# Kernel tuning notes

Hardware: AMD Instinct MI355X
Metric: run time of the kernel (lower is better)

## Reference

```python
import jax, jax.numpy as jnp
import numpy as np


def _conv1x1(x, w, b):
    # x: [B, Cin, H, W], w: [Cout, Cin], b: [Cout]
    return jnp.einsum('bchw,oc->bohw', x, w) + b[None, :, None, None]


def setup_inputs() -> dict:
    key = jax.random.key(0)
    ks = jax.random.split(key, 9)
    B, C, H, W = 32, 512, 32, 32
    Cout, dn = 512, 512
    s_in = 1.0 / np.sqrt(C)
    s_out = 1.0 / np.sqrt(Cout)
    return {
        'x': jax.random.normal(ks[0], (B, C, H, W), jnp.float32),
        'wA': jax.random.uniform(ks[1], (Cout, C), jnp.float32, -s_in, s_in),
        'bA': jax.random.uniform(ks[2], (Cout,), jnp.float32, -s_in, s_in),
        'wB': jax.random.uniform(ks[3], (dn, C), jnp.float32, -s_in, s_in),
        'bB': jax.random.uniform(ks[4], (dn,), jnp.float32, -s_in, s_in),
        'wV': jax.random.uniform(ks[5], (dn, C), jnp.float32, -s_in, s_in),
        'bV': jax.random.uniform(ks[6], (dn,), jnp.float32, -s_in, s_in),
        'wR': jax.random.uniform(ks[7], (Cout, Cout), jnp.float32, -s_out, s_out),
        'bR': jax.random.uniform(ks[8], (Cout,), jnp.float32, -s_out, s_out),
    }


def reference(x, wA, bA, wB, bB, wV, bV, wR, bR):
    Bsz, C, H, W = x.shape
    Cout = wA.shape[0]
    A = _conv1x1(x, wA, bA).reshape(Bsz, Cout, H * W)          # [B, Cout, N]
    Bm = _conv1x1(x, wB, bB).reshape(Bsz, wB.shape[0], H * W)  # [B, dn, N]
    Vm = _conv1x1(x, wV, bV).reshape(Bsz, wV.shape[0], H * W)  # [B, dn, N]
    attn_maps = jax.nn.softmax(Bm, axis=-1)                    # softmax over spatial
    attn_vectors = jax.nn.softmax(Vm, axis=-1)                 # softmax over spatial
    glob_desc = jnp.einsum('bcn,bdn->bcd', A, attn_maps)       # [B, Cout, dn]
    Z = jnp.einsum('bcd,bdn->bcn', glob_desc, attn_vectors)    # [B, Cout, N]
    Z = Z.reshape(Bsz, Cout, H, W)
    Z = _conv1x1(Z, wR, bR)
    return Z
```

## Files before the change

kernel.cpp:

```cpp
#include <hip/hip_runtime.h>
#include <stdint.h>

typedef unsigned short u16;
typedef __bf16  bf16x8 __attribute__((ext_vector_type(8)));
typedef float   f32x4  __attribute__((ext_vector_type(4)));

__device__ __forceinline__ u16 f2bf(float f) {
    union { float f; unsigned u; } c; c.f = f;
    unsigned r = c.u + 0x7fffu + ((c.u >> 16) & 1u);
    return (u16)(r >> 16);
}
__device__ __forceinline__ float bf2f(u16 b) {
    union { unsigned u; float f; } c; c.u = ((unsigned)b) << 16; return c.f;
}

__device__ __forceinline__ void g2l16(const u16* g, u16* l) {
    __builtin_amdgcn_global_load_lds(
        (__attribute__((address_space(1))) void*)(uintptr_t)g,
        (__attribute__((address_space(3))) void*)(uint32_t)(uintptr_t)l,
        16, 0, 0);
}

template <int TM, bool HAS_BIAS, bool OUT_F32, bool EPI>
__device__ __forceinline__ void gemm_core(
    const u16* __restrict__ Ab, const u16* __restrict__ Bb, void* __restrict__ C,
    const float* __restrict__ bias, int N, int K, long cbase, int m0, int n0,
    const float* __restrict__ svec, const float* __restrict__ wRbA)
{
    constexpr int MI = TM / 32;
    constexpr int NA = TM / 32;
    __shared__ __align__(16) u16 As[TM * 64];
    __shared__ __align__(16) u16 Bs[128 * 64];

    const int t = threadIdx.x;
    const int w = t >> 6, lane = t & 63;
    const int wr = w >> 1, wc = w & 1;

    f32x4 acc[MI][4];
    const f32x4 zero = {0.f, 0.f, 0.f, 0.f};
#pragma unroll
    for (int i = 0; i < MI; ++i)
#pragma unroll
        for (int j = 0; j < 4; ++j) acc[i][j] = zero;

    int  aslot[NA]; long aoff[NA];
#pragma unroll
    for (int i = 0; i < NA; ++i) {
        const int s   = i * 256 + t;
        const int row = s >> 3;
        const int col = ((s & 7) ^ (row & 7)) * 8;
        aslot[i] = s * 8;
        aoff[i]  = (long)(m0 + row) * K + col;
    }
    int  bslot[4]; long boff[4];
#pragma unroll
    for (int i = 0; i < 4; ++i) {
        const int s   = i * 256 + t;
        const int row = s >> 3;
        const int col = ((s & 7) ^ (row & 7)) * 8;
        bslot[i] = s * 8;
        boff[i]  = (long)(n0 + row) * K + col;
    }

    const int fr = lane & 15;
    const int q  = lane >> 4;
    const int o0 = ((q ^ (fr & 7)) * 8);
    const u16* fa = &As[(wr * (TM / 2) + fr) * 64];
    const u16* fb = &Bs[(wc * 64 + fr) * 64];

    for (int k0 = 0; k0 < K; k0 += 64) {
#pragma unroll
        for (int i = 0; i < NA; ++i) g2l16(Ab + aoff[i] + k0, &As[aslot[i]]);
#pragma unroll
        for (int i = 0; i < 4; ++i)  g2l16(Bb + boff[i] + k0, &Bs[bslot[i]]);
        __syncthreads();

#pragma unroll
        for (int kh = 0; kh < 2; ++kh) {
            const int o = o0 ^ (kh * 32);
            bf16x8 af[MI], bv[4];
#pragma unroll
            for (int mi = 0; mi < MI; ++mi) af[mi] = *(const bf16x8*)(fa + mi * 1024 + o);
#pragma unroll
            for (int ni = 0; ni < 4; ++ni)  bv[ni] = *(const bf16x8*)(fb + ni * 1024 + o);
#pragma unroll
            for (int mi = 0; mi < MI; ++mi)
#pragma unroll
                for (int ni = 0; ni < 4; ++ni)
                    acc[mi][ni] = __builtin_amdgcn_mfma_f32_16x16x32_bf16(
                        af[mi], bv[ni], acc[mi][ni], 0, 0, 0);
        }
        __syncthreads();
    }

    const int ccol  = n0 + wc * 64 + fr;
    const int crow0 = m0 + wr * (TM / 2) + (lane >> 4) * 4;
    float se[4];
    if (EPI) {
#pragma unroll
        for (int ni = 0; ni < 4; ++ni) se[ni] = svec[ccol + ni * 16];
    }
#pragma unroll
    for (int mi = 0; mi < MI; ++mi) {
#pragma unroll
        for (int r = 0; r < 4; ++r) {
            const int row = crow0 + mi * 16 + r;
            float add = HAS_BIAS ? bias[row] : 0.f;
            float rk  = EPI ? wRbA[row] : 0.f;
#pragma unroll
            for (int ni = 0; ni < 4; ++ni) {
                float v = acc[mi][ni][r] + add;
                if (EPI) v += rk * se[ni];
                const long idx = cbase + (long)row * N + ccol + ni * 16;
                if (OUT_F32) ((float*)C)[idx] = v;
                else         ((u16*)C)[idx]   = f2bf(v);
            }
        }
    }
}

template <int TM, bool HAS_BIAS, bool OUT_F32>
__global__ __launch_bounds__(256) void gemm_nt(
    const u16* __restrict__ A, const u16* __restrict__ B, void* __restrict__ C,
    const float* __restrict__ bias, int N, int K, long sA, long sB, long sC)
{
    const int bz = blockIdx.z;
    gemm_core<TM, HAS_BIAS, OUT_F32, false>(
        A + (long)bz * sA, B + (long)bz * sB, C, bias, N, K,
        (long)bz * sC, blockIdx.y * TM, blockIdx.x * 128, nullptr, nullptr);
}

template <int TM, bool HAS_BIAS, bool OUT_F32, bool EPI>
__global__ __launch_bounds__(256) void gemm_nt_swz(
    const u16* __restrict__ A, const u16* __restrict__ B, void* __restrict__ C,
    const float* __restrict__ bias, int N, int K, long sA, long sB, long sC,
    int bxn, int bpb, const float* __restrict__ s_all,
    const float* __restrict__ wRbA)
{
    const int blk  = blockIdx.x;
    const int xcd  = blk & 7;
    const int slot = blk >> 3;
    const int b    = xcd + 8 * (slot / bpb);
    const int wi   = slot % bpb;
    const int bx   = wi % bxn;
    const int by   = wi / bxn;
    gemm_core<TM, HAS_BIAS, OUT_F32, EPI>(
        A + (long)b * sA, B + (long)b * sB, C, bias, N, K,
        (long)b * sC, by * TM, bx * 128,
        EPI ? s_all + (long)b * 1024 : nullptr, wRbA);
}

__global__ __launch_bounds__(512) void gemm2_y(
    const u16* __restrict__ A,
    const u16* __restrict__ B,
    u16* __restrict__ C,
    const float* __restrict__ bias)
{
    constexpr int K    = 512;
    constexpr int NT   = K / 32;
    constexpr int AREG = 256 * 32;
    constexpr int BUFQ = 2 * AREG;
    __shared__ __align__(16) u16 lds[4 * BUFQ];

    const int blk  = blockIdx.x;
    const int xcd  = blk & 7;
    const int slot = blk >> 3;
    const int bz   = xcd + 8 * (slot / 24);
    const int wi   = slot % 24;
    const int m0   = (wi >> 2) * 256;
    const int n0   = (wi & 3) * 256;

    const u16* Ab = A;
    const u16* Bb = B + (long)bz * (1024 * 512);
    u16*       Cb = C + (long)bz * ((long)1536 * 1024);

    const int t    = threadIdx.x;
    const int w    = t >> 6, lane = t & 63;
    const int wr   = w >> 2, wc = w & 3;
    const int fr   = lane & 15, q = lane >> 4;

    int  aslot[2]; long agoff[2], bgoff[2];
#pragma unroll
    for (int i = 0; i < 2; ++i) {
        const int ci  = i * 512 + t;
        const int row = ci >> 2;
        const int gc  = (ci & 3) ^ ((row >> 1) & 3);
        aslot[i] = ci * 8;
        agoff[i] = (long)(m0 + row) * K + gc * 8;
        bgoff[i] = (long)(n0 + row) * K + gc * 8;
    }

    const int rchunk = (q ^ ((fr >> 1) & 3)) * 8;
    const int abase  = (wr * 128 + fr) * 32 + rchunk;
    const int bbase  = (wc * 64  + fr) * 32 + rchunk;

    f32x4 acc[8][4];
    const f32x4 zero = {0.f, 0.f, 0.f, 0.f};
#pragma unroll
    for (int i = 0; i < 8; ++i)
#pragma unroll
        for (int j = 0; j < 4; ++j) acc[i][j] = zero;

#pragma unroll
    for (int i = 0; i < 2; ++i) g2l16(Ab + agoff[i],        &lds[aslot[i]]);
#pragma unroll
    for (int i = 0; i < 2; ++i) g2l16(Bb + bgoff[i],        &lds[AREG + aslot[i]]);
#pragma unroll
    for (int i = 0; i < 2; ++i) g2l16(Ab + agoff[i] + 32,   &lds[BUFQ + aslot[i]]);
#pragma unroll
    for (int i = 0; i < 2; ++i) g2l16(Bb + bgoff[i] + 32,   &lds[BUFQ + AREG + aslot[i]]);
    asm volatile("s_waitcnt vmcnt(4)" ::: "memory");
    __builtin_amdgcn_s_barrier();
    asm volatile("" ::: "memory");

#pragma unroll
    for (int kt = 0; kt < NT; ++kt) {
        const u16* Abuf = &lds[(kt & 3) * BUFQ];
        const u16* Bbuf = Abuf + AREG;
        u16* dst = &lds[((kt + 2) & 3) * BUFQ];
        const long kg = (long)(kt + 2) * 32;

        bf16x8 av[8], bv[4];
#pragma unroll
        for (int mi = 0; mi < 8; ++mi) av[mi] = *(const bf16x8*)(Abuf + abase + mi * 512);
#pragma unroll
        for (int ni = 0; ni < 4; ++ni) bv[ni] = *(const bf16x8*)(Bbuf + bbase + ni * 512);
        if (kt + 2 < NT) {
#pragma unroll
            for (int i = 0; i < 2; ++i) g2l16(Ab + agoff[i] + kg, dst + aslot[i]);
#pragma unroll
            for (int i = 0; i < 2; ++i) g2l16(Bb + bgoff[i] + kg, dst + AREG + aslot[i]);
        }
#pragma unroll
        for (int mi = 0; mi < 8; ++mi)
#pragma unroll
            for (int ni = 0; ni < 4; ++ni)
                acc[mi][ni] = __builtin_amdgcn_mfma_f32_16x16x32_bf16(
                    av[mi], bv[ni], acc[mi][ni], 0, 0, 0);

        if (kt + 1 < NT) {
            if (kt + 2 < NT) asm volatile("s_waitcnt vmcnt(4)" ::: "memory");
            else             asm volatile("s_waitcnt vmcnt(0)" ::: "memory");
            __builtin_amdgcn_s_barrier();
            asm volatile("" ::: "memory");
        }
    }

    const int ccol  = n0 + wc * 64 + fr;
    const int crow0 = m0 + wr * 128 + q * 4;
#pragma unroll
    for (int mi = 0; mi < 8; ++mi) {
#pragma unroll
        for (int r = 0; r < 4; ++r) {
            const int row = crow0 + mi * 16 + r;
            const float add = bias[row];
#pragma unroll
            for (int ni = 0; ni < 4; ++ni)
                Cb[(long)row * 1024 + ccol + ni * 16] = f2bf(acc[mi][ni][r] + add);
        }
    }
}

__global__ __launch_bounds__(256) void cast_transpose_x(
    const float* __restrict__ in, u16* __restrict__ out)
{
    __shared__ u16 tile[64][68];
    const int bz = blockIdx.z;
    const float* ip = in  + (long)bz * (512 * 1024);
    u16*         op = out + (long)bz * (1024 * 512);
    const int c0 = blockIdx.x * 64;
    const int r0 = blockIdx.y * 64;
    const int tx = threadIdx.x & 15;
    const int ty = threadIdx.x >> 4;
#pragma unroll
    for (int p = 0; p < 4; ++p) {
        const int row = ty + 16 * p;
        float4 v = *(const float4*)(ip + (long)(r0 + row) * 1024 + c0 + 4 * tx);
        ushort4 o;
        o.x = f2bf(v.x); o.y = f2bf(v.y); o.z = f2bf(v.z); o.w = f2bf(v.w);
        *(ushort4*)&tile[row][4 * tx] = o;
    }
    __syncthreads();
#pragma unroll
    for (int p = 0; p < 4; ++p) {
        const int orow = ty + 16 * p;
        ushort4 o;
        o.x = tile[4 * tx + 0][orow];
        o.y = tile[4 * tx + 1][orow];
        o.z = tile[4 * tx + 2][orow];
        o.w = tile[4 * tx + 3][orow];
        *(ushort4*)&op[(long)(c0 + orow) * 512 + r0 + 4 * tx] = o;
    }
}

__global__ __launch_bounds__(256) void transpose_colsum(
    const u16* __restrict__ in, u16* __restrict__ out, float* __restrict__ s,
    long sIn, long sOut, const float2* __restrict__ stats_all)
{
    __shared__ u16 tile[64][68];
    const int bz = blockIdx.z;
    const u16* ip = in  + (long)bz * sIn;
    u16*       op = out + (long)bz * sOut;
    const int c0 = blockIdx.x * 64;
    const int r0 = blockIdx.y * 64;
    const int t  = threadIdx.x;
    const int tx = t & 15;
    const int ty = t >> 4;
#pragma unroll
    for (int p = 0; p < 4; ++p) {
        const int row = ty + 16 * p;
        const float2 st = stats_all[(long)bz * 1024 + 512 + r0 + row];
        ushort4 v = *(const ushort4*)(ip + (long)(r0 + row) * 1024 + c0 + 4 * tx);
        ushort4 o;
        o.x = f2bf(__expf(bf2f(v.x) - st.x) * st.y);
        o.y = f2bf(__expf(bf2f(v.y) - st.x) * st.y);
        o.z = f2bf(__expf(bf2f(v.z) - st.x) * st.y);
        o.w = f2bf(__expf(bf2f(v.w) - st.x) * st.y);
        *(ushort4*)&tile[row][4 * tx] = o;
    }
    __syncthreads();
#pragma unroll
    for (int p = 0; p < 4; ++p) {
        const int orow = ty + 16 * p;
        ushort4 o;
        o.x = tile[4 * tx + 0][orow];
        o.y = tile[4 * tx + 1][orow];
        o.z = tile[4 * tx + 2][orow];
        o.w = tile[4 * tx + 3][orow];
        *(ushort4*)&op[(long)(c0 + orow) * 512 + r0 + 4 * tx] = o;
    }
    if (t < 64) {
        float a = 0.f;
#pragma unroll 8
        for (int d = 0; d < 64; ++d) a += bf2f(tile[d][t]);
        atomicAdd(&s[(long)bz * 1024 + c0 + t], a);
    }
}

__global__ __launch_bounds__(256) void prep_weights(
    const float* __restrict__ wA, const float* __restrict__ wB,
    const float* __restrict__ wV, const float* __restrict__ wR,
    const float* __restrict__ bA, const float* __restrict__ bB,
    const float* __restrict__ bV,
    u16* __restrict__ Wcat, u16* __restrict__ wRb, u16* __restrict__ wAtb,
    float* __restrict__ bcat, float* __restrict__ wRbA,
    float* __restrict__ svec)
{
    const int blk = blockIdx.x;
    if (blk < 4103) {
        const int tid = blk * 256 + threadIdx.x;
        if (tid < 262144) {
            Wcat[262144 + tid] = f2bf(wB[tid]);
        } else if (tid < 524288) {
            Wcat[262144 + tid] = f2bf(wV[tid - 262144]);
        } else if (tid < 786432) {
            wRb[tid - 524288] = f2bf(wR[tid - 524288]);
        } else if (tid < 1048576) {
            const int i = tid - 786432;
            wAtb[(i & 511) * 512 + (i >> 9)] = f2bf(wA[i]);
        } else if (tid < 1048576 + 1536) {
            const int j = tid - 1048576;
            bcat[j] = (j < 512) ? 0.f : (j < 1024) ? bB[j - 512] : bV[j - 1024];
        }
    } else if (blk < 4231) {
        const int o    = (blk - 4103) * 4 + (threadIdx.x >> 6);
        const int lane = threadIdx.x & 63;
        float a = 0.f;
#pragma unroll
        for (int c = lane; c < 512; c += 64) a += wR[o * 512 + c] * bA[c];
#pragma unroll
        for (int off = 32; off > 0; off >>= 1) a += __shfl_down(a, off);
        if (lane == 0) wRbA[o] = a;
    } else {
        const int idx = (blk - 4231) * 256 + threadIdx.x;
        svec[idx] = 0.f;
    }
}

__global__ __launch_bounds__(256) void softmax_apply(
    const u16* __restrict__ Y, u16* __restrict__ attnM,
    float2* __restrict__ stats)
{
    const int j  = blockIdx.x;
    const int bz = blockIdx.y;
    const u16* row = Y + (long)bz * (1536 * 1024) + (long)(512 + j) * 1024;
    const int t = threadIdx.x;
    ushort4 u = ((const ushort4*)row)[t];
    float v0 = bf2f(u.x), v1 = bf2f(u.y), v2 = bf2f(u.z), v3 = bf2f(u.w);

    float m = fmaxf(fmaxf(v0, v1), fmaxf(v2, v3));
#pragma unroll
    for (int off = 32; off > 0; off >>= 1) m = fmaxf(m, __shfl_down(m, off));

    __shared__ float smax[4];
    __shared__ float ssum[4];
    const int w = t >> 6, lane = t & 63;
    if (lane == 0) smax[w] = m;
    __syncthreads();
    m = fmaxf(fmaxf(smax[0], smax[1]), fmaxf(smax[2], smax[3]));

    float e0 = __expf(v0 - m), e1 = __expf(v1 - m);
    float e2 = __expf(v2 - m), e3 = __expf(v3 - m);
    float s = e0 + e1 + e2 + e3;
#pragma unroll
    for (int off = 32; off > 0; off >>= 1) s += __shfl_down(s, off);
    if (lane == 0) ssum[w] = s;
    __syncthreads();
    const float inv = 1.0f / (ssum[0] + ssum[1] + ssum[2] + ssum[3]);

    if (j < 512) {
        ushort4 o;
        o.x = f2bf(e0 * inv); o.y = f2bf(e1 * inv);
        o.z = f2bf(e2 * inv); o.w = f2bf(e3 * inv);
        ((ushort4*)(attnM + (long)bz * (512 * 1024) + (long)j * 1024))[t] = o;
    } else if (t == 0) {
        float2 r; r.x = m; r.y = inv;
        stats[(long)bz * 1024 + j] = r;
    }
}

extern "C" void kernel_launch(void* const* d_in, const int* in_sizes, int n_in,
                              void* d_out, int out_size, void* d_ws, size_t ws_size,
                              hipStream_t stream)
{
    (void)in_sizes; (void)n_in; (void)out_size; (void)ws_size;
    const float* x  = (const float*)d_in[0];
    const float* wA = (const float*)d_in[1];
    const float* bA = (const float*)d_in[2];
    const float* wB = (const float*)d_in[3];
    const float* bB = (const float*)d_in[4];
    const float* wV = (const float*)d_in[5];
    const float* bV = (const float*)d_in[6];
    const float* wR = (const float*)d_in[7];
    const float* bR = (const float*)d_in[8];
    float* out = (float*)d_out;

    const int B = 32;
    const long sY = (long)1536 * 1024;

    char* p = (char*)d_ws;
    u16*   Y    = (u16*)p;   p += (long)B * sY * 2;
    u16*   H    = (u16*)p;   p += (long)B * 512 * 512 * 2;
    u16*   Wcat = (u16*)p;   p += (long)1536 * 512 * 2;
    u16*   wRb  = (u16*)p;   p += (long)512 * 512 * 2;
    u16*   wAtb = (u16*)p;   p += (long)512 * 512 * 2;
    float* bcat = (float*)p; p += 1536 * 4;
    float* svec = (float*)p; p += (long)B * 1024 * 4;
    float* wRbA = (float*)p; p += 512 * 4;
    float2* rowstats = (float2*)p; p += (long)B * 1024 * sizeof(float2);

    u16* Xt    = (u16*)d_out;
    u16* attnM = (u16*)d_out + (long)16777216;
    u16* Vt = Y;

    cast_transpose_x<<<dim3(16, 8, B), 256, 0, stream>>>(x, Xt);
    prep_weights<<<dim3(4359), 256, 0, stream>>>(wA, wB, wV, wR, bA, bB, bV,
                                                 Wcat, wRb, wAtb, bcat, wRbA, svec);

    gemm_nt<128, false, false><<<dim3(4, 4, 1), 256, 0, stream>>>(
        wRb, wAtb, Wcat, nullptr, 512, 512, 0, 0, 0);

    gemm2_y<<<dim3(768), 512, 0, stream>>>(Wcat, Xt, Y, bcat);

    softmax_apply<<<dim3(1024, B), 256, 0, stream>>>(Y, attnM, rowstats);

    gemm_nt_swz<128, false, false, false><<<dim3(512), 256, 0, stream>>>(
        Y, attnM, H, nullptr, 512, 1024,
        sY, (long)512 * 1024, (long)512 * 512, 4, 16, nullptr, nullptr);

    transpose_colsum<<<dim3(16, 8, B), 256, 0, stream>>>(
        Y + (long)1024 * 1024, Vt, svec, sY, sY, rowstats);

    gemm_nt_swz<128, true, true, true><<<dim3(1024), 256, 0, stream>>>(
        H, Vt, out, bR, 1024, 512, (long)512 * 512, sY, (long)512 * 1024,
        8, 32, svec, wRbA);
}
```

Measured before the change: 297.3 us.

## Fuse softmax exp and row sums into projection GEMM epilogue, drop softmax kernel

The projection GEMM epilogue now applies exp to the B and V rows without max subtraction and accumulates row sums with atomics. The standalone softmax kernel and its attention-map buffer are removed. Normalisation moves into the next GEMM's epilogue as a per-column scale, and into transpose_colsum as a per-row scale. This removes a full read and write pass over the B/V activations. The cost is unstabilised exp, which risks overflow for large logits and adds atomics in the epilogue.

```diff
diff --git a/kernel.cpp b/kernel.cpp
--- a/kernel.cpp
+++ b/kernel.cpp
@@ -21,11 +21,12 @@
         16, 0, 0);
 }
 
-template <int TM, bool HAS_BIAS, bool OUT_F32, bool EPI>
+template <int TM, bool HAS_BIAS, bool OUT_F32, bool EPI, bool CSCALE>
 __device__ __forceinline__ void gemm_core(
     const u16* __restrict__ Ab, const u16* __restrict__ Bb, void* __restrict__ C,
     const float* __restrict__ bias, int N, int K, long cbase, int m0, int n0,
-    const float* __restrict__ svec, const float* __restrict__ wRbA)
+    const float* __restrict__ svec, const float* __restrict__ wRbA,
+    const float* __restrict__ rs)
 {
     constexpr int MI = TM / 32;
     constexpr int NA = TM / 32;
@@ -95,10 +96,15 @@
 
     const int ccol  = n0 + wc * 64 + fr;
     const int crow0 = m0 + wr * (TM / 2) + (lane >> 4) * 4;
-    float se[4];
+    float se[4], sc[4];
     if (EPI) {
 #pragma unroll
         for (int ni = 0; ni < 4; ++ni) se[ni] = svec[ccol + ni * 16];
+    }
+    if (CSCALE) {
+#pragma unroll
+        for (int ni = 0; ni < 4; ++ni)
+            sc[ni] = 1.0f / (rs[ccol + ni * 16] * rs[512 + ccol + ni * 16]);
     }
 #pragma unroll
     for (int mi = 0; mi < MI; ++mi) {
@@ -110,7 +116,8 @@
 #pragma unroll
             for (int ni = 0; ni < 4; ++ni) {
                 float v = acc[mi][ni][r] + add;
-                if (EPI) v += rk * se[ni];
+                if (CSCALE) v *= sc[ni];
+                if (EPI)    v += rk * se[ni];
                 const long idx = cbase + (long)row * N + ccol + ni * 16;
                 if (OUT_F32) ((float*)C)[idx] = v;
                 else         ((u16*)C)[idx]   = f2bf(v);
@@ -125,17 +132,17 @@
     const float* __restrict__ bias, int N, int K, long sA, long sB, long sC)
 {
     const int bz = blockIdx.z;
-    gemm_core<TM, HAS_BIAS, OUT_F32, false>(
+    gemm_core<TM, HAS_BIAS, OUT_F32, false, false>(
         A + (long)bz * sA, B + (long)bz * sB, C, bias, N, K,
-        (long)bz * sC, blockIdx.y * TM, blockIdx.x * 128, nullptr, nullptr);
-}
-
-template <int TM, bool HAS_BIAS, bool OUT_F32, bool EPI>
+        (long)bz * sC, blockIdx.y * TM, blockIdx.x * 128, nullptr, nullptr, nullptr);
+}
+
+template <int TM, bool HAS_BIAS, bool OUT_F32, bool EPI, bool CSCALE>
 __global__ __launch_bounds__(256) void gemm_nt_swz(
     const u16* __restrict__ A, const u16* __restrict__ B, void* __restrict__ C,
     const float* __restrict__ bias, int N, int K, long sA, long sB, long sC,
     int bxn, int bpb, const float* __restrict__ s_all,
-    const float* __restrict__ wRbA)
+    const float* __restrict__ wRbA, const float* __restrict__ rs_all)
 {
     const int blk  = blockIdx.x;
     const int xcd  = blk & 7;
@@ -144,17 +151,19 @@
     const int wi   = slot % bpb;
     const int bx   = wi % bxn;
     const int by   = wi / bxn;
-    gemm_core<TM, HAS_BIAS, OUT_F32, EPI>(
+    gemm_core<TM, HAS_BIAS, OUT_F32, EPI, CSCALE>(
         A + (long)b * sA, B + (long)b * sB, C, bias, N, K,
         (long)b * sC, by * TM, bx * 128,
-        EPI ? s_all + (long)b * 1024 : nullptr, wRbA);
+        EPI ? s_all + (long)b * 1024 : nullptr, wRbA,
+        CSCALE ? rs_all + (long)b * 1024 : nullptr);
 }
 
 __global__ __launch_bounds__(512) void gemm2_y(
     const u16* __restrict__ A,
     const u16* __restrict__ B,
     u16* __restrict__ C,
-    const float* __restrict__ bias)
+    const float* __restrict__ bias,
+    float* __restrict__ rowsum)
 {
     constexpr int K    = 512;
     constexpr int NT   = K / 32;
@@ -248,15 +257,28 @@
 
     const int ccol  = n0 + wc * 64 + fr;
     const int crow0 = m0 + wr * 128 + q * 4;
+    const bool sm = (m0 >= 512);
+    float* rsb = rowsum + (long)bz * 1024;
 #pragma unroll
     for (int mi = 0; mi < 8; ++mi) {
 #pragma unroll
         for (int r = 0; r < 4; ++r) {
             const int row = crow0 + mi * 16 + r;
             const float add = bias[row];
-#pragma unroll
-            for (int ni = 0; ni < 4; ++ni)
-                Cb[(long)row * 1024 + ccol + ni * 16] = f2bf(acc[mi][ni][r] + add);
+            float rsum = 0.f;
+#pragma unroll
+            for (int ni = 0; ni < 4; ++ni) {
+                float v = acc[mi][ni][r] + add;
+                if (sm) { v = __expf(v); rsum += v; }
+                Cb[(long)row * 1024 + ccol + ni * 16] = f2bf(v);
+            }
+            if (sm) {
+                rsum += __shfl_xor(rsum, 1);
+                rsum += __shfl_xor(rsum, 2);
+                rsum += __shfl_xor(rsum, 4);
+                rsum += __shfl_xor(rsum, 8);
+                if (fr == 0) atomicAdd(&rsb[row - 512], rsum);
+            }
         }
     }
 }
@@ -295,9 +317,10 @@
 
 __global__ __launch_bounds__(256) void transpose_colsum(
     const u16* __restrict__ in, u16* __restrict__ out, float* __restrict__ s,
-    long sIn, long sOut, const float2* __restrict__ stats_all)
+    long sIn, long sOut, const float* __restrict__ rowsum)
 {
     __shared__ u16 tile[64][68];
+    __shared__ float sinv[64];
     const int bz = blockIdx.z;
     const u16* ip = in  + (long)bz * sIn;
     u16*       op = out + (long)bz * sOut;
@@ -306,17 +329,12 @@
     const int t  = threadIdx.x;
     const int tx = t & 15;
     const int ty = t >> 4;
+    if (t < 64) sinv[t] = 1.0f / rowsum[(long)bz * 1024 + 512 + r0 + t];
 #pragma unroll
     for (int p = 0; p < 4; ++p) {
         const int row = ty + 16 * p;
-        const float2 st = stats_all[(long)bz * 1024 + 512 + r0 + row];
         ushort4 v = *(const ushort4*)(ip + (long)(r0 + row) * 1024 + c0 + 4 * tx);
-        ushort4 o;
-        o.x = f2bf(__expf(bf2f(v.x) - st.x) * st.y);
-        o.y = f2bf(__expf(bf2f(v.y) - st.x) * st.y);
-        o.z = f2bf(__expf(bf2f(v.z) - st.x) * st.y);
-        o.w = f2bf(__expf(bf2f(v.w) - st.x) * st.y);
-        *(ushort4*)&tile[row][4 * tx] = o;
+        *(ushort4*)&tile[row][4 * tx] = v;
     }
     __syncthreads();
 #pragma unroll
@@ -332,7 +350,7 @@
     if (t < 64) {
         float a = 0.f;
 #pragma unroll 8
-        for (int d = 0; d < 64; ++d) a += bf2f(tile[d][t]);
+        for (int d = 0; d < 64; ++d) a += bf2f(tile[d][t]) * sinv[d];
         atomicAdd(&s[(long)bz * 1024 + c0 + t], a);
     }
 }
@@ -344,7 +362,7 @@
     const float* __restrict__ bV,
     u16* __restrict__ Wcat, u16* __restrict__ wRb, u16* __restrict__ wAtb,
     float* __restrict__ bcat, float* __restrict__ wRbA,
-    float* __restrict__ svec)
+    float* __restrict__ svec, float* __restrict__ rowsum)
 {
     const int blk = blockIdx.x;
     if (blk < 4103) {
@@ -371,51 +389,10 @@
 #pragma unroll
         for (int off = 32; off > 0; off >>= 1) a += __shfl_down(a, off);
         if (lane == 0) wRbA[o] = a;
+    } else if (blk < 4359) {
+        svec[(blk - 4231) * 256 + threadIdx.x] = 0.f;
     } else {
-        const int idx = (blk - 4231) * 256 + threadIdx.x;
-        svec[idx] = 0.f;
-    }
-}
-
-__global__ __launch_bounds__(256) void softmax_apply(
-    const u16* __restrict__ Y, u16* __restrict__ attnM,
-    float2* __restrict__ stats)
-{
-    const int j  = blockIdx.x;
-    const int bz = blockIdx.y;
-    const u16* row = Y + (long)bz * (1536 * 1024) + (long)(512 + j) * 1024;
-    const int t = threadIdx.x;
-    ushort4 u = ((const ushort4*)row)[t];
-    float v0 = bf2f(u.x), v1 = bf2f(u.y), v2 = bf2f(u.z), v3 = bf2f(u.w);
-
-    float m = fmaxf(fmaxf(v0, v1), fmaxf(v2, v3));
-#pragma unroll
-    for (int off = 32; off > 0; off >>= 1) m = fmaxf(m, __shfl_down(m, off));
-
-    __shared__ float smax[4];
-    __shared__ float ssum[4];
-    const int w = t >> 6, lane = t & 63;
-    if (lane == 0) smax[w] = m;
-    __syncthreads();
-    m = fmaxf(fmaxf(smax[0], smax[1]), fmaxf(smax[2], smax[3]));
-
-    float e0 = __expf(v0 - m), e1 = __expf(v1 - m);
-    float e2 = __expf(v2 - m), e3 = __expf(v3 - m);
-    float s = e0 + e1 + e2 + e3;
-#pragma unroll
-    for (int off = 32; off > 0; off >>= 1) s += __shfl_down(s, off);
-    if (lane == 0) ssum[w] = s;
-    __syncthreads();
-    const float inv = 1.0f / (ssum[0] + ssum[1] + ssum[2] + ssum[3]);
-
-    if (j < 512) {
-        ushort4 o;
-        o.x = f2bf(e0 * inv); o.y = f2bf(e1 * inv);
-        o.z = f2bf(e2 * inv); o.w = f2bf(e3 * inv);
-        ((ushort4*)(attnM + (long)bz * (512 * 1024) + (long)j * 1024))[t] = o;
-    } else if (t == 0) {
-        float2 r; r.x = m; r.y = inv;
-        stats[(long)bz * 1024 + j] = r;
+        rowsum[(blk - 4359) * 256 + threadIdx.x] = 0.f;
     }
 }
 
@@ -447,31 +424,29 @@
     float* bcat = (float*)p; p += 1536 * 4;
     float* svec = (float*)p; p += (long)B * 1024 * 4;
     float* wRbA = (float*)p; p += 512 * 4;
-    float2* rowstats = (float2*)p; p += (long)B * 1024 * sizeof(float2);
-
-    u16* Xt    = (u16*)d_out;
-    u16* attnM = (u16*)d_out + (long)16777216;
+    float* rowsum = (float*)p; p += (long)B * 1024 * 4;
+
+    u16* Xt = (u16*)d_out;
     u16* Vt = Y;
 
     cast_transpose_x<<<dim3(16, 8, B), 256, 0, stream>>>(x, Xt);
-    prep_weights<<<dim3(4359), 256, 0, stream>>>(wA, wB, wV, wR, bA, bB, bV,
-                                                 Wcat, wRb, wAtb, bcat, wRbA, svec);
+    prep_weights<<<dim3(4487), 256, 0, stream>>>(wA, wB, wV, wR, bA, bB, bV,
+                                                 Wcat, wRb, wAtb, bcat, wRbA,
+                                                 svec, rowsum);
 
     gemm_nt<128, false, false><<<dim3(4, 4, 1), 256, 0, stream>>>(
         wRb, wAtb, Wcat, nullptr, 512, 512, 0, 0, 0);
 
-    gemm2_y<<<dim3(768), 512, 0, stream>>>(Wcat, Xt, Y, bcat);
-
-    softmax_apply<<<dim3(1024, B), 256, 0, stream>>>(Y, attnM, rowstats);
-
-    gemm_nt_swz<128, false, false, false><<<dim3(512), 256, 0, stream>>>(
-        Y, attnM, H, nullptr, 512, 1024,
-        sY, (long)512 * 1024, (long)512 * 512, 4, 16, nullptr, nullptr);
+    gemm2_y<<<dim3(768), 512, 0, stream>>>(Wcat, Xt, Y, bcat, rowsum);
+
+    gemm_nt_swz<128, false, false, false, true><<<dim3(512), 256, 0, stream>>>(
+        Y, Y + (long)512 * 1024, H, nullptr, 512, 1024,
+        sY, sY, (long)512 * 512, 4, 16, nullptr, nullptr, rowsum);
 
     transpose_colsum<<<dim3(16, 8, B), 256, 0, stream>>>(
-        Y + (long)1024 * 1024, Vt, svec, sY, sY, rowstats);
-
-    gemm_nt_swz<128, true, true, true><<<dim3(1024), 256, 0, stream>>>(
+        Y + (long)1024 * 1024, Vt, svec, sY, sY, rowsum);
+
+    gemm_nt_swz<128, true, true, true, false><<<dim3(1024), 256, 0, stream>>>(
         H, Vt, out, bR, 1024, 512, (long)512 * 512, sY, (long)512 * 1024,
-        8, 32, svec, wRbA);
-}
+        8, 32, svec, wRbA, nullptr);
+}
```

Measured after the change: 300.8 us. About the same (+1.2%).
